# Kernel optimization log

Hardware: AMD Instinct MI355X
Metric: run time of the kernel (lower is better)

## Reference

```python
import jax, jax.numpy as jnp
import numpy as np

B, NB, NA, D, PF = 16384, 8, 16, 128, 1
IN_DIM = D + NA * D + D  # basis + flattened sf + task = 2304
QK_DIM = D * 3 * PF      # 384
V_DIM = D * PF           # 128


def rbf_similarity(x, y):
    # RBF kernel over the feature axis: exp(-0.5 * ||x - y||^2)
    return jnp.exp(-0.5 * jnp.sum((x - y) ** 2, axis=-1))


def setup_inputs() -> dict:
    key = jax.random.key(0)
    ks = jax.random.split(key, 9)
    basis = jax.random.normal(ks[0], (B, NB, D), dtype=jnp.float32)
    sf_all = jax.random.normal(ks[1], (B, NB, NA, D), dtype=jnp.float32)
    task = jax.random.normal(ks[2], (B, NB, D), dtype=jnp.float32)
    mask = (jax.random.uniform(ks[3], (B, NB, D * PF)) > 0.5).astype(jnp.float32)
    s_in = 1.0 / np.sqrt(IN_DIM)
    s_v = 1.0 / np.sqrt(D)
    Wq = jax.random.normal(ks[4], (IN_DIM, QK_DIM), dtype=jnp.float32) * s_in
    Wk = jax.random.normal(ks[5], (IN_DIM, QK_DIM), dtype=jnp.float32) * s_in
    bk = jnp.zeros((QK_DIM,), dtype=jnp.float32)
    Wv = jax.random.normal(ks[6], (D, V_DIM), dtype=jnp.float32) * s_v
    bv = jnp.zeros((V_DIM,), dtype=jnp.float32)
    return {"basis_features_all": basis, "sf_all": sf_all, "task": task, "mask": mask,
            "Wq": Wq, "Wk": Wk, "bk": bk, "Wv": Wv, "bv": bv}


def reference(basis_features_all, sf_all, task, mask, Wq, Wk, bk, Wv, bv):
    b = sf_all.shape[0]
    sf_all_r = jnp.reshape(sf_all, (b, NB, NA * D))          # (B, NB, NA*D)
    sf_first_r = sf_all_r[:, :1, :]                          # (B, 1, NA*D)
    task = jax.lax.stop_gradient(task)
    task_n = task / jnp.linalg.norm(task, ord=2, axis=-1, keepdims=True)

    # RBF similarity side-branch between consecutive beakers
    bst = jnp.concatenate([basis_features_all, sf_all_r, task_n], axis=-1)  # (B, NB, IN_DIM)
    sim = rbf_similarity(bst[:, :-1, :], bst[:, 1:, :]).mean(axis=0)        # (NB-1,)

    bf_first = basis_features_all[:, :1, :]
    bf_rest = jax.lax.stop_gradient(basis_features_all[:, 1:, :])
    bf_all = jnp.concatenate([bf_first, bf_rest], axis=1)

    q_in = jnp.concatenate([bf_first, sf_first_r, task_n[:, :1, :]], axis=-1)  # (B, 1, IN_DIM)
    query = q_in @ Wq                                                          # (B, 1, QK)
    k_in = jnp.concatenate([bf_all, sf_all_r, task_n], axis=-1)                # (B, NB, IN_DIM)
    keys = k_in @ Wk + bk                                                      # (B, NB, QK)
    values = sf_all @ Wv + bv                                                  # (B, NB, NA, V)

    mask_rep = jnp.repeat(mask, 3, axis=-1)                                    # (B, NB, QK)
    keys_masked = keys * mask_rep
    values_masked = values

    attn_logits = jnp.matmul(query, jnp.swapaxes(keys_masked, -2, -1)) / jnp.sqrt(jnp.float32(D * PF))
    attn_logits = jnp.where(attn_logits == 0, -1e9, attn_logits)               # zero-mask trick
    attention_weights = jax.nn.softmax(attn_logits, axis=-1)                   # (B, 1, NB)

    attended_sf = jnp.einsum('bna,baqf->bnqf', attention_weights, values_masked)  # (B, 1, NA, V)
    task_first = task[:, 0, :]                                                    # (B, D)
    q_1 = jnp.einsum('bi,bnji->bj', task_first, attended_sf)                      # (B, NA)
    return (q_1, attended_sf, attn_logits, attention_weights, keys_masked, values_masked, sim)
```

## Files before the change

kernel.cpp:

```cpp
#include <hip/hip_runtime.h>
#include <hip/hip_bf16.h>
#include <math.h>

static constexpr size_t OFF_ATT = 262144;
static constexpr size_t OFF_LOG = 33816576;
static constexpr size_t OFF_W   = 33947648;
static constexpr size_t OFF_KM  = 34078720;
static constexpr size_t OFF_VM  = 84410368;
static constexpr size_t OFF_SIM = 352845824;

typedef short bf16x8 __attribute__((ext_vector_type(8)));
typedef float f32x4 __attribute__((ext_vector_type(4)));

__device__ inline unsigned short f2bf(float f) {
  union { float f; unsigned u; } x; x.f = f;
  unsigned r = x.u + 0x7FFFu + ((x.u >> 16) & 1u);
  return (unsigned short)(r >> 16);
}

__device__ inline float wave_sum(float v) {
#pragma unroll
  for (int o = 32; o > 0; o >>= 1) v += __shfl_xor(v, o, 64);
  return v;
}

__global__ void norm_kernel(const float* __restrict__ task, float* __restrict__ invn,
                            float* __restrict__ simo) {
  int idx = blockIdx.x * 4 + (threadIdx.x >> 6);
  int lane = threadIdx.x & 63;
  float t0 = task[(size_t)idx * 128 + lane];
  float t1 = task[(size_t)idx * 128 + 64 + lane];
  float s = wave_sum(t0 * t0 + t1 * t1);
  if (lane == 0) invn[idx] = rsqrtf(s);
  if (blockIdx.x == 0 && threadIdx.x < 7) simo[threadIdx.x] = 0.0f;
}

__global__ void wprep_t(const float* __restrict__ W, unsigned short* __restrict__ WT,
                        int K, int N) {
  int ntn = N >> 6;
  int kt = blockIdx.x / ntn, nt = blockIdx.x % ntn;
  int k0 = kt * 64, n0 = nt * 64;
  __shared__ float t[64][65];
  int tid = threadIdx.x;
  int r = tid >> 2, c0 = (tid & 3) * 16;
#pragma unroll
  for (int q = 0; q < 4; ++q) {
    float4 v = *(const float4*)(W + (size_t)(k0 + r) * N + n0 + c0 + q * 4);
    t[r][c0 + q * 4 + 0] = v.x; t[r][c0 + q * 4 + 1] = v.y;
    t[r][c0 + q * 4 + 2] = v.z; t[r][c0 + q * 4 + 3] = v.w;
  }
  __syncthreads();
  int n = tid >> 2, kc0 = (tid & 3) * 16;
#pragma unroll
  for (int q = 0; q < 4; ++q) {
    int kc = kc0 + q * 4;
    ushort4 o = make_ushort4(f2bf(t[kc + 0][n]), f2bf(t[kc + 1][n]),
                             f2bf(t[kc + 2][n]), f2bf(t[kc + 3][n]));
    *(ushort4*)(WT + (size_t)(n0 + n) * K + k0 + kc) = o;
  }
}

__global__ __launch_bounds__(576) void abuild_sim(const float* __restrict__ basis,
                                                  const float* __restrict__ sf,
                                                  const float* __restrict__ task,
                                                  const float* __restrict__ invn,
                                                  unsigned short* __restrict__ Abf,
                                                  float* __restrict__ simo) {
  int b = blockIdx.x;
  int f = threadIdx.x;
  size_t row0 = (size_t)b * 8;
  float4 v[8];
#pragma unroll
  for (int n = 0; n < 8; ++n) {
    size_t row = row0 + n;
    float4 x;
    if (f < 32)       x = *(const float4*)(basis + row * 128 + f * 4);
    else if (f < 544) x = *(const float4*)(sf + row * 2048 + (f - 32) * 4);
    else {
      x = *(const float4*)(task + row * 128 + (f - 544) * 4);
      float s = invn[row];
      x.x *= s; x.y *= s; x.z *= s; x.w *= s;
    }
    v[n] = x;
    ushort4 o = make_ushort4(f2bf(x.x), f2bf(x.y), f2bf(x.z), f2bf(x.w));
    *(ushort4*)(Abf + row * 2304 + f * 4) = o;
  }
  float s7[7];
#pragma unroll
  for (int n = 1; n < 8; ++n) {
    float dx = v[n].x - v[n - 1].x, dy = v[n].y - v[n - 1].y;
    float dz = v[n].z - v[n - 1].z, dw = v[n].w - v[n - 1].w;
    s7[n - 1] = dx * dx + dy * dy + dz * dz + dw * dw;
  }
  __shared__ float red[9][7];
  int wid = threadIdx.x >> 6, lane = threadIdx.x & 63;
#pragma unroll
  for (int i = 0; i < 7; ++i) {
    float p = wave_sum(s7[i]);
    if (lane == 0) red[wid][i] = p;
  }
  __syncthreads();
  if (threadIdx.x < 7) {
    float s = 0.f;
#pragma unroll
    for (int w = 0; w < 9; ++w) s += red[w][threadIdx.x];
    atomicAdd(&simo[threadIdx.x], expf(-0.5f * s) * (1.0f / 16384.0f));
  }
}

template <int MODE>
__global__ __launch_bounds__(256) void qk_gemm(const unsigned short* __restrict__ Abf,
                                               const unsigned short* __restrict__ WT,
                                               const float* __restrict__ bias,
                                               const float* __restrict__ mask,
                                               float* __restrict__ outp) {
  __shared__ unsigned short As[2 * 4096];
  __shared__ unsigned short Bs[2 * 4096];
  int nwg = gridDim.x, per = nwg >> 3;
  int bid = blockIdx.x;
  int swz = (bid & 7) * per + (bid >> 3);
  int mt = swz / 3, nt = swz - mt * 3;
  int tid = threadIdx.x;
  int wave = tid >> 6, lane = tid & 63;
  int wr = wave >> 1, wc = wave & 1;
  int m0g = mt * 128, n0g = nt * 128;

  int c_lo = wave * 128 + lane;
  int row_q0 = c_lo >> 2, kc_q0 = ((c_lo & 3) ^ ((row_q0 >> 1) & 3)) * 8;
  int c_hi = c_lo + 64;
  int row_q1 = c_hi >> 2, kc_q1 = ((c_hi & 3) ^ ((row_q1 >> 1) & 3)) * 8;
  size_t ga_q0 = (MODE == 1) ? (size_t)(m0g + row_q0) * 8 : (size_t)(m0g + row_q0);
  size_t ga_q1 = (MODE == 1) ? (size_t)(m0g + row_q1) * 8 : (size_t)(m0g + row_q1);
  const unsigned short* ag0 = Abf + ga_q0 * 2304 + kc_q0;
  const unsigned short* ag1 = Abf + ga_q1 * 2304 + kc_q1;
  const unsigned short* bg0 = WT + (size_t)(n0g + row_q0) * 2304 + kc_q0;
  const unsigned short* bg1 = WT + (size_t)(n0g + row_q1) * 2304 + kc_q1;
  int ldsoff0 = wave * 1024;
  int ldsoff1 = ldsoff0 + 512;

#define STAGE(ks, cur)                                                                   \
  do {                                                                                   \
    int _k0 = (ks) * 32;                                                                 \
    unsigned short* _a = As + (cur) * 4096;                                              \
    unsigned short* _b = Bs + (cur) * 4096;                                              \
    __builtin_amdgcn_global_load_lds(                                                    \
        (const __attribute__((address_space(1))) void*)(ag0 + _k0),                      \
        (__attribute__((address_space(3))) void*)(_a + ldsoff0), 16, 0, 0);              \
    __builtin_amdgcn_global_load_lds(                                                    \
        (const __attribute__((address_space(1))) void*)(ag1 + _k0),                      \
        (__attribute__((address_space(3))) void*)(_a + ldsoff1), 16, 0, 0);              \
    __builtin_amdgcn_global_load_lds(                                                    \
        (const __attribute__((address_space(1))) void*)(bg0 + _k0),                      \
        (__attribute__((address_space(3))) void*)(_b + ldsoff0), 16, 0, 0);              \
    __builtin_amdgcn_global_load_lds(                                                    \
        (const __attribute__((address_space(1))) void*)(bg1 + _k0),                      \
        (__attribute__((address_space(3))) void*)(_b + ldsoff1), 16, 0, 0);              \
  } while (0)

  f32x4 acc[4][4];
#pragma unroll
  for (int i = 0; i < 4; ++i)
#pragma unroll
    for (int j = 0; j < 4; ++j) acc[i][j] = (f32x4)(0.f);

  int la = lane & 15;
  int sl = (((lane >> 4) ^ ((la >> 1) & 3))) * 8;

  STAGE(0, 0);
  __syncthreads();
  int cur = 0;
  for (int ks = 0; ks < 72; ++ks) {
    if (ks < 71) STAGE(ks + 1, cur ^ 1);
    const unsigned short* aL = As + cur * 4096;
    const unsigned short* bL = Bs + cur * 4096;
    bf16x8 af[4], bf[4];
#pragma unroll
    for (int mi = 0; mi < 4; ++mi)
      af[mi] = *(const bf16x8*)(aL + (wr * 64 + mi * 16 + la) * 32 + sl);
#pragma unroll
    for (int ni = 0; ni < 4; ++ni)
      bf[ni] = *(const bf16x8*)(bL + (wc * 64 + ni * 16 + la) * 32 + sl);
#pragma unroll
    for (int mi = 0; mi < 4; ++mi)
#pragma unroll
      for (int ni = 0; ni < 4; ++ni)
        acc[mi][ni] = __builtin_amdgcn_mfma_f32_16x16x32_bf16(af[mi], bf[ni], acc[mi][ni], 0, 0, 0);
    __syncthreads();
    cur ^= 1;
  }
#undef STAGE

  int rq = lane >> 4;
#pragma unroll
  for (int mi = 0; mi < 4; ++mi) {
#pragma unroll
    for (int ni = 0; ni < 4; ++ni) {
      int colg = nt * 128 + wc * 64 + ni * 16 + la;
#pragma unroll
      for (int j = 0; j < 4; ++j) {
        int rowg = mt * 128 + wr * 64 + mi * 16 + rq * 4 + j;
        float v = acc[mi][ni][j];
        if (MODE == 0)
          v = (v + bias[colg]) * mask[(size_t)rowg * 128 + (unsigned)colg / 3u];
        outp[(size_t)rowg * 384 + colg] = v;
      }
    }
  }
}

__global__ __launch_bounds__(256) void attn_kernel4(const float* __restrict__ query,
                                                    const float* __restrict__ km,
                                                    float* __restrict__ logits,
                                                    float* __restrict__ wts) {
  int w = threadIdx.x >> 6, lane = threadIdx.x & 63;
  int b = blockIdx.x * 4 + w;
  float q[6];
#pragma unroll
  for (int j = 0; j < 6; ++j) q[j] = query[(size_t)b * 384 + lane + 64 * j];
  float lg[8];
#pragma unroll
  for (int n = 0; n < 8; ++n) {
    const float* kr = km + ((size_t)b * 8 + n) * 384;
    float p = 0.f;
#pragma unroll
    for (int j = 0; j < 6; ++j) p = fmaf(q[j], kr[lane + 64 * j], p);
    p = wave_sum(p);
    float l = p * 0.08838834764831845f;
    lg[n] = (l == 0.0f) ? -1e9f : l;
  }
  float m = lg[0];
#pragma unroll
  for (int i = 1; i < 8; ++i) m = fmaxf(m, lg[i]);
  float ex[8], s = 0.f;
#pragma unroll
  for (int i = 0; i < 8; ++i) { ex[i] = expf(lg[i] - m); s += ex[i]; }
  float inv = 1.0f / s;
  if (lane < 8) {
    float lv = lg[0], ev = ex[0];
#pragma unroll
    for (int i = 1; i < 8; ++i)
      if (lane == i) { lv = lg[i]; ev = ex[i]; }
    logits[(size_t)b * 8 + lane] = lv;
    wts[(size_t)b * 8 + lane] = ev * inv;
  }
}

template <int ABF>
__global__ __launch_bounds__(256) void v_gemm_attend(const float* __restrict__ sf,
                                                     const unsigned short* __restrict__ Abf,
                                                     const float* __restrict__ Wv,
                                                     const unsigned short* __restrict__ WvT,
                                                     const float* __restrict__ bv,
                                                     const float* __restrict__ wts,
                                                     const float* __restrict__ task,
                                                     float* __restrict__ vm,
                                                     float* __restrict__ att,
                                                     float* __restrict__ q1) {
  __shared__ unsigned short As[2 * 4096];
  __shared__ unsigned short Bs[128 * 136];
  float* attL = (float*)As;
  int bid = blockIdx.x;
  int swz = (bid & 7) * 2048 + (bid >> 3);
  int b = swz;
  size_t m0 = (size_t)swz * 128;
  int tid = threadIdx.x;
  int wave = tid >> 6, lane = tid & 63;
  int wr = wave >> 1, wc = wave & 1;
  int r = tid >> 1, h = tid & 1;
  int la = lane & 15, lkq = lane >> 4;
  int sl = ((lkq ^ ((la >> 1) & 3))) * 8;

  if (ABF) {
#pragma unroll
    for (int q = 0; q < 8; ++q) {
      bf16x8 v = *(const bf16x8*)(WvT + (size_t)r * 128 + h * 64 + q * 8);
      *(bf16x8*)(Bs + r * 136 + h * 64 + q * 8) = v;
    }
  } else {
#pragma unroll
    for (int q = 0; q < 16; ++q) {
      int flat = q * 256 + tid;
      int k = flat >> 5;
      int n4 = (flat & 31) * 4;
      float4 v = *(const float4*)(Wv + (size_t)k * 128 + n4);
      Bs[(n4 + 0) * 136 + k] = f2bf(v.x);
      Bs[(n4 + 1) * 136 + k] = f2bf(v.y);
      Bs[(n4 + 2) * 136 + k] = f2bf(v.z);
      Bs[(n4 + 3) * 136 + k] = f2bf(v.w);
    }
  }

  const unsigned short *ap0 = nullptr, *ap1 = nullptr;
  int ldsA0 = wave * 1024, ldsA1 = ldsA0 + 512;
  if (ABF) {
    int p0 = wave * 128 + lane;
    int tr0 = p0 >> 2, ds0 = (p0 & 3) ^ ((tr0 >> 1) & 3);
    int p1 = p0 + 64;
    int tr1 = p1 >> 2, ds1 = (p1 & 3) ^ ((tr1 >> 1) & 3);
    ap0 = Abf + ((size_t)b * 8 + (tr0 >> 4)) * 2304 + 128 + (tr0 & 15) * 128 + ds0 * 8;
    ap1 = Abf + ((size_t)b * 8 + (tr1 >> 4)) * 2304 + 128 + (tr1 & 15) * 128 + ds1 * 8;
    __builtin_amdgcn_global_load_lds(
        (const __attribute__((address_space(1))) void*)(ap0),
        (__attribute__((address_space(3))) void*)(As + ldsA0), 16, 0, 0);
    __builtin_amdgcn_global_load_lds(
        (const __attribute__((address_space(1))) void*)(ap1),
        (__attribute__((address_space(3))) void*)(As + ldsA1), 16, 0, 0);
  }

  f32x4 acc[4][4];
#pragma unroll
  for (int i = 0; i < 4; ++i)
#pragma unroll
    for (int j = 0; j < 4; ++j) acc[i][j] = (f32x4)(0.f);

  if (ABF) __syncthreads();

  int cur = 0;
  for (int ks = 0; ks < 4; ++ks) {
    int k0 = ks * 32;
    if (ABF) {
      if (ks < 3) {
        __builtin_amdgcn_global_load_lds(
            (const __attribute__((address_space(1))) void*)(ap0 + k0 + 32),
            (__attribute__((address_space(3))) void*)(As + (cur ^ 1) * 4096 + ldsA0), 16, 0, 0);
        __builtin_amdgcn_global_load_lds(
            (const __attribute__((address_space(1))) void*)(ap1 + k0 + 32),
            (__attribute__((address_space(3))) void*)(As + (cur ^ 1) * 4096 + ldsA1), 16, 0, 0);
      }
    } else {
      const float* ap = sf + (m0 + r) * 128 + k0 + h * 16;
      float4 v0 = *(const float4*)(ap);
      float4 v1 = *(const float4*)(ap + 4);
      float4 v2 = *(const float4*)(ap + 8);
      float4 v3 = *(const float4*)(ap + 12);
      ushort4 p0 = make_ushort4(f2bf(v0.x), f2bf(v0.y), f2bf(v0.z), f2bf(v0.w));
      ushort4 p1 = make_ushort4(f2bf(v1.x), f2bf(v1.y), f2bf(v1.z), f2bf(v1.w));
      ushort4 p2 = make_ushort4(f2bf(v2.x), f2bf(v2.y), f2bf(v2.z), f2bf(v2.w));
      ushort4 p3 = make_ushort4(f2bf(v3.x), f2bf(v3.y), f2bf(v3.z), f2bf(v3.w));
      *(ushort4*)(As + r * 40 + h * 16)      = p0;
      *(ushort4*)(As + r * 40 + h * 16 + 4)  = p1;
      *(ushort4*)(As + r * 40 + h * 16 + 8)  = p2;
      *(ushort4*)(As + r * 40 + h * 16 + 12) = p3;
      __syncthreads();
    }
    const unsigned short* aL = ABF ? (As + cur * 4096) : As;
    bf16x8 af[4], bfr[4];
#pragma unroll
    for (int mi = 0; mi < 4; ++mi) {
      int rowl = wr * 64 + mi * 16 + la;
      af[mi] = ABF ? *(const bf16x8*)(aL + rowl * 32 + sl)
                   : *(const bf16x8*)(aL + rowl * 40 + lkq * 8);
    }
#pragma unroll
    for (int ni = 0; ni < 4; ++ni)
      bfr[ni] = *(const bf16x8*)(Bs + (wc * 64 + ni * 16 + la) * 136 + k0 + lkq * 8);
#pragma unroll
    for (int mi = 0; mi < 4; ++mi)
#pragma unroll
      for (int ni = 0; ni < 4; ++ni)
        acc[mi][ni] = __builtin_amdgcn_mfma_f32_16x16x32_bf16(af[mi], bfr[ni], acc[mi][ni], 0, 0, 0);
    __syncthreads();
    cur ^= 1;
  }

  float w4[4];
#pragma unroll
  for (int mi = 0; mi < 4; ++mi) w4[mi] = wts[(size_t)b * 8 + wr * 4 + mi];
  float pacc[4][4];
#pragma unroll
  for (int ni = 0; ni < 4; ++ni)
#pragma unroll
    for (int j = 0; j < 4; ++j) pacc[ni][j] = 0.f;
#pragma unroll
  for (int mi = 0; mi < 4; ++mi) {
#pragma unroll
    for (int ni = 0; ni < 4; ++ni) {
      int colg = wc * 64 + ni * 16 + la;
      float bb = bv[colg];
#pragma unroll
      for (int j = 0; j < 4; ++j) {
        size_t rowg = m0 + wr * 64 + mi * 16 + lkq * 4 + j;
        float v = acc[mi][ni][j] + bb;
        vm[rowg * 128 + colg] = v;
        pacc[ni][j] = fmaf(w4[mi], v, pacc[ni][j]);
      }
    }
  }
  if (wr == 0) {
#pragma unroll
    for (int ni = 0; ni < 4; ++ni)
#pragma unroll
      for (int j = 0; j < 4; ++j)
        attL[(lkq * 4 + j) * 132 + wc * 64 + ni * 16 + la] = pacc[ni][j];
  }
  __syncthreads();
  if (wr == 1) {
#pragma unroll
    for (int ni = 0; ni < 4; ++ni)
#pragma unroll
      for (int j = 0; j < 4; ++j)
        attL[(lkq * 4 + j) * 132 + wc * 64 + ni * 16 + la] += pacc[ni][j];
  }
  __syncthreads();
#pragma unroll
  for (int i = 0; i < 2; ++i) {
    int fidx = tid + i * 256;
    int a = fidx >> 5, c = (fidx & 31) * 4;
    f32x4 vv = *(const f32x4*)(attL + a * 132 + c);
    *(f32x4*)(att + (size_t)b * 2048 + a * 128 + c) = vv;
  }
  for (int j = wave; j < 16; j += 4) {
    float p = task[(size_t)b * 1024 + lane] * attL[j * 132 + lane]
            + task[(size_t)b * 1024 + 64 + lane] * attL[j * 132 + 64 + lane];
    p = wave_sum(p);
    if (lane == 0) q1[(size_t)b * 16 + j] = p;
  }
}

extern "C" void kernel_launch(void* const* d_in, const int* in_sizes, int n_in,
                              void* d_out, int out_size, void* d_ws, size_t ws_size,
                              hipStream_t stream) {
  const float* basis = (const float*)d_in[0];
  const float* sf    = (const float*)d_in[1];
  const float* task  = (const float*)d_in[2];
  const float* mask  = (const float*)d_in[3];
  const float* Wq    = (const float*)d_in[4];
  const float* Wk    = (const float*)d_in[5];
  const float* bk    = (const float*)d_in[6];
  const float* Wv    = (const float*)d_in[7];
  const float* bv    = (const float*)d_in[8];

  float* out  = (float*)d_out;
  float* q1   = out;
  float* att  = out + OFF_ATT;
  float* logi = out + OFF_LOG;
  float* wts  = out + OFF_W;
  float* km   = out + OFF_KM;
  float* vm   = out + OFF_VM;
  float* simo = out + OFF_SIM;

  constexpr size_t WS_NEED = 603979776ull + 1769472ull + 1769472ull + 32768ull +
                             25165824ull + 524288ull;
  bool usews = ws_size >= WS_NEED;

  unsigned short *Abf, *WkT, *WqT, *WvT = nullptr;
  float *query, *invn;
  if (usews) {
    unsigned char* ws = (unsigned char*)d_ws;
    Abf   = (unsigned short*)ws;
    WkT   = (unsigned short*)(ws + 603979776ull);
    WqT   = (unsigned short*)(ws + 605749248ull);
    WvT   = (unsigned short*)(ws + 607518720ull);
    query = (float*)(ws + 607551488ull);
    invn  = (float*)(ws + 632717312ull);
  } else {
    query = att;
    invn  = att + 6291456;
    WkT   = (unsigned short*)(att + 6422528);
    WqT   = WkT + 884736;
    Abf   = (unsigned short*)vm;
  }

  norm_kernel<<<32768, 256, 0, stream>>>(task, invn, simo);
  wprep_t<<<216, 256, 0, stream>>>(Wk, WkT, 2304, 384);
  wprep_t<<<216, 256, 0, stream>>>(Wq, WqT, 2304, 384);
  if (usews) wprep_t<<<4, 256, 0, stream>>>(Wv, WvT, 128, 128);
  abuild_sim<<<16384, 576, 0, stream>>>(basis, sf, task, invn, Abf, simo);
  qk_gemm<0><<<3072, 256, 0, stream>>>(Abf, WkT, bk, mask, km);
  qk_gemm<1><<<384, 256, 0, stream>>>(Abf, WqT, nullptr, nullptr, query);
  attn_kernel4<<<4096, 256, 0, stream>>>(query, km, logi, wts);
  if (usews)
    v_gemm_attend<1><<<16384, 256, 0, stream>>>(sf, Abf, Wv, WvT, bv, wts, task, vm, att, q1);
  else
    v_gemm_attend<0><<<16384, 256, 0, stream>>>(sf, Abf, Wv, WvT, bv, wts, task, vm, att, q1);
}
```

Before: 1.283 ms.

## Fuse input conversion and similarity into keys GEMM, drop full bf16 A buffer

A new keys_build kernel loads the fp32 basis, sf and normalized task rows directly, converts them to bf16 in LDS and runs the key GEMM in the same pass, so the separate abuild_sim kernel no longer writes and re-reads the full bf16 A matrix. It also produces a compact bf16 copy of sf for the V GEMM and the query rows for the Q GEMM, spreading these writes across the three column-tile blocks. The RBF similarity is accumulated from the bf16 tiles already in LDS, which lowers its precision. Each of the three column tiles now re-reads the fp32 inputs, relying on the swizzle and L2 to soften that cost.

Result: slower. 1.509 ms (+17.7%).

```diff
diff --git a/kernel.cpp b/kernel.cpp
--- a/kernel.cpp
+++ b/kernel.cpp
@@ -16,6 +16,9 @@
   union { float f; unsigned u; } x; x.f = f;
   unsigned r = x.u + 0x7FFFu + ((x.u >> 16) & 1u);
   return (unsigned short)(r >> 16);
+}
+__device__ inline float bf2f(unsigned short v) {
+  union { unsigned u; float f; } x; x.u = ((unsigned)v) << 16; return x.f;
 }
 
 __device__ inline float wave_sum(float v) {
@@ -57,6 +60,172 @@
     ushort4 o = make_ushort4(f2bf(t[kc + 0][n]), f2bf(t[kc + 1][n]),
                              f2bf(t[kc + 2][n]), f2bf(t[kc + 3][n]));
     *(ushort4*)(WT + (size_t)(n0 + n) * K + k0 + kc) = o;
+  }
+}
+
+__global__ __launch_bounds__(256) void keys_build(
+    const float* __restrict__ basis, const float* __restrict__ sf,
+    const float* __restrict__ task, const float* __restrict__ invn,
+    const unsigned short* __restrict__ WkT, const float* __restrict__ bias,
+    const float* __restrict__ mask, float* __restrict__ km,
+    unsigned short* __restrict__ sfbf, unsigned short* __restrict__ qbf,
+    float* __restrict__ simo) {
+  __shared__ unsigned short As[2 * 5120];
+  __shared__ unsigned short Bs[2 * 4096];
+  int bid = blockIdx.x;
+  int swz = (bid & 7) * 384 + (bid >> 3);
+  int mt = swz / 3, nt = swz - mt * 3;
+  int tid = threadIdx.x;
+  int wave = tid >> 6, lane = tid & 63;
+  int wr = wave >> 1, wc = wave & 1;
+  int m0g = mt * 128, n0g = nt * 128;
+  int la = lane & 15, lkq = lane >> 4;
+  int sl = ((lkq ^ ((la >> 1) & 3))) * 8;
+
+  int c_lo = wave * 128 + lane;
+  int brow0 = c_lo >> 2, bkc0 = ((c_lo & 3) ^ ((brow0 >> 1) & 3)) * 8;
+  int c_hi = c_lo + 64;
+  int brow1 = c_hi >> 2, bkc1 = ((c_hi & 3) ^ ((brow1 >> 1) & 3)) * 8;
+  const unsigned short* bg0 = WkT + (size_t)(n0g + brow0) * 2304 + bkc0;
+  const unsigned short* bg1 = WkT + (size_t)(n0g + brow1) * 2304 + bkc1;
+  int ldsB0 = wave * 1024, ldsB1 = ldsB0 + 512;
+
+#define STAGE_B(ks, cb)                                                        \
+  do {                                                                         \
+    __builtin_amdgcn_global_load_lds(                                          \
+        (const __attribute__((address_space(1))) void*)(bg0 + (ks) * 32),      \
+        (__attribute__((address_space(3))) void*)(Bs + (cb) * 4096 + ldsB0),   \
+        16, 0, 0);                                                             \
+    __builtin_amdgcn_global_load_lds(                                          \
+        (const __attribute__((address_space(1))) void*)(bg1 + (ks) * 32),      \
+        (__attribute__((address_space(3))) void*)(Bs + (cb) * 4096 + ldsB1),   \
+        16, 0, 0);                                                             \
+  } while (0)
+
+  int rbase = tid >> 3, c4 = tid & 7;
+  float ivq[4];
+#pragma unroll
+  for (int q = 0; q < 4; ++q) ivq[q] = invn[m0g + rbase + 32 * q];
+  bool qrow = ((rbase & 7) == 0);
+  bool simblk = (nt == 0);
+
+  float4 av[4];
+
+  auto LOADA = [&](int k0) {
+#pragma unroll
+    for (int q = 0; q < 4; ++q) {
+      size_t R = (size_t)(m0g + rbase + 32 * q);
+      int k = k0 + c4 * 4;
+      const float* p;
+      if (k0 < 128)       p = basis + R * 128 + k;
+      else if (k0 < 2176) p = sf + R * 2048 + (k - 128);
+      else                p = task + R * 128 + (k - 2176);
+      float4 x = *(const float4*)p;
+      if (k0 >= 2176) { x.x *= ivq[q]; x.y *= ivq[q]; x.z *= ivq[q]; x.w *= ivq[q]; }
+      av[q] = x;
+    }
+  };
+
+  auto CVTW = [&](int cb, int kt) {
+    unsigned short* aL = As + cb * 5120;
+    bool wr_this = (nt == (kt % 3));
+    int k0 = kt * 32;
+#pragma unroll
+    for (int q = 0; q < 4; ++q) {
+      int row = rbase + 32 * q;
+      ushort4 o = make_ushort4(f2bf(av[q].x), f2bf(av[q].y), f2bf(av[q].z), f2bf(av[q].w));
+      *(ushort4*)(aL + row * 40 + c4 * 4) = o;
+      if (wr_this) {
+        size_t R = (size_t)(m0g + row);
+        int k = k0 + c4 * 4;
+        if (k0 >= 128 && k0 < 2176)
+          *(ushort4*)(sfbf + R * 2048 + (k - 128)) = o;
+        if (qrow)
+          *(ushort4*)(qbf + (R >> 3) * 2304 + k) = o;
+      }
+    }
+  };
+
+  f32x4 acc[4][4];
+#pragma unroll
+  for (int i = 0; i < 4; ++i)
+#pragma unroll
+    for (int j = 0; j < 4; ++j) acc[i][j] = (f32x4)(0.f);
+
+  float sa = 0.f;
+  int pr = tid >> 1, hh = tid & 1;
+  bool prok = ((pr & 7) != 7);
+
+  LOADA(0);
+  STAGE_B(0, 0);
+  CVTW(0, 0);
+  __syncthreads();
+
+  int cur = 0;
+  for (int ks = 0; ks < 72; ++ks) {
+    if (ks < 71) {
+      LOADA((ks + 1) * 32);
+      STAGE_B(ks + 1, cur ^ 1);
+    }
+    {
+      const unsigned short* aL = As + cur * 5120;
+      const unsigned short* bL = Bs + cur * 4096;
+      bf16x8 af[4], bfr[4];
+#pragma unroll
+      for (int mi = 0; mi < 4; ++mi)
+        af[mi] = *(const bf16x8*)(aL + (wr * 64 + mi * 16 + la) * 40 + lkq * 8);
+#pragma unroll
+      for (int ni = 0; ni < 4; ++ni)
+        bfr[ni] = *(const bf16x8*)(bL + (wc * 64 + ni * 16 + la) * 32 + sl);
+#pragma unroll
+      for (int mi = 0; mi < 4; ++mi)
+#pragma unroll
+        for (int ni = 0; ni < 4; ++ni)
+          acc[mi][ni] = __builtin_amdgcn_mfma_f32_16x16x32_bf16(af[mi], bfr[ni], acc[mi][ni], 0, 0, 0);
+    }
+    if (simblk && prok) {
+      const unsigned short* a0 = As + cur * 5120 + pr * 40 + hh * 16;
+      bf16x8 x0 = *(const bf16x8*)(a0);
+      bf16x8 x1 = *(const bf16x8*)(a0 + 8);
+      bf16x8 y0 = *(const bf16x8*)(a0 + 40);
+      bf16x8 y1 = *(const bf16x8*)(a0 + 48);
+#pragma unroll
+      for (int j = 0; j < 8; ++j) {
+        float d0 = bf2f((unsigned short)x0[j]) - bf2f((unsigned short)y0[j]);
+        sa = fmaf(d0, d0, sa);
+        float d1 = bf2f((unsigned short)x1[j]) - bf2f((unsigned short)y1[j]);
+        sa = fmaf(d1, d1, sa);
+      }
+    }
+    if (ks < 71) CVTW(cur ^ 1, ks + 1);
+    __syncthreads();
+    cur ^= 1;
+  }
+#undef STAGE_B
+
+  int rq = lane >> 4;
+#pragma unroll
+  for (int mi = 0; mi < 4; ++mi) {
+#pragma unroll
+    for (int ni = 0; ni < 4; ++ni) {
+      int colg = n0g + wc * 64 + ni * 16 + la;
+#pragma unroll
+      for (int j = 0; j < 4; ++j) {
+        int rowg = m0g + wr * 64 + mi * 16 + rq * 4 + j;
+        float v = (acc[mi][ni][j] + bias[colg]) * mask[(size_t)rowg * 128 + (unsigned)colg / 3u];
+        km[(size_t)rowg * 384 + colg] = v;
+      }
+    }
+  }
+
+  if (simblk) {
+    float* sarr = (float*)Bs;
+    sarr[tid] = sa;
+    __syncthreads();
+    if (hh == 0 && prok) {
+      float s = sarr[tid] + sarr[tid + 1];
+      atomicAdd(&simo[pr & 7], expf(-0.5f * s) * (1.0f / 16384.0f));
+    }
   }
 }
 
@@ -129,8 +298,8 @@
   int row_q0 = c_lo >> 2, kc_q0 = ((c_lo & 3) ^ ((row_q0 >> 1) & 3)) * 8;
   int c_hi = c_lo + 64;
   int row_q1 = c_hi >> 2, kc_q1 = ((c_hi & 3) ^ ((row_q1 >> 1) & 3)) * 8;
-  size_t ga_q0 = (MODE == 1) ? (size_t)(m0g + row_q0) * 8 : (size_t)(m0g + row_q0);
-  size_t ga_q1 = (MODE == 1) ? (size_t)(m0g + row_q1) * 8 : (size_t)(m0g + row_q1);
+  size_t ga_q0 = (MODE == 2) ? (size_t)(m0g + row_q0) * 8 : (size_t)(m0g + row_q0);
+  size_t ga_q1 = (MODE == 2) ? (size_t)(m0g + row_q1) * 8 : (size_t)(m0g + row_q1);
   const unsigned short* ag0 = Abf + ga_q0 * 2304 + kc_q0;
   const unsigned short* ag1 = Abf + ga_q1 * 2304 + kc_q1;
   const unsigned short* bg0 = WT + (size_t)(n0g + row_q0) * 2304 + kc_q0;
@@ -247,7 +416,7 @@
 
 template <int ABF>
 __global__ __launch_bounds__(256) void v_gemm_attend(const float* __restrict__ sf,
-                                                     const unsigned short* __restrict__ Abf,
+                                                     const unsigned short* __restrict__ sfbf,
                                                      const float* __restrict__ Wv,
                                                      const unsigned short* __restrict__ WvT,
                                                      const float* __restrict__ bv,
@@ -297,8 +466,8 @@
     int tr0 = p0 >> 2, ds0 = (p0 & 3) ^ ((tr0 >> 1) & 3);
     int p1 = p0 + 64;
     int tr1 = p1 >> 2, ds1 = (p1 & 3) ^ ((tr1 >> 1) & 3);
-    ap0 = Abf + ((size_t)b * 8 + (tr0 >> 4)) * 2304 + 128 + (tr0 & 15) * 128 + ds0 * 8;
-    ap1 = Abf + ((size_t)b * 8 + (tr1 >> 4)) * 2304 + 128 + (tr1 & 15) * 128 + ds1 * 8;
+    ap0 = sfbf + ((size_t)b * 8 + (tr0 >> 4)) * 2048 + (tr0 & 15) * 128 + ds0 * 8;
+    ap1 = sfbf + ((size_t)b * 8 + (tr1 >> 4)) * 2048 + (tr1 & 15) * 128 + ds1 * 8;
     __builtin_amdgcn_global_load_lds(
         (const __attribute__((address_space(1))) void*)(ap0),
         (__attribute__((address_space(3))) void*)(As + ldsA0), 16, 0, 0);
@@ -439,38 +608,51 @@
   float* vm   = out + OFF_VM;
   float* simo = out + OFF_SIM;
 
-  constexpr size_t WS_NEED = 603979776ull + 1769472ull + 1769472ull + 32768ull +
-                             25165824ull + 524288ull;
+  constexpr size_t O_SFBF = 0;
+  constexpr size_t O_QBF  = 536870912ull;
+  constexpr size_t O_WKT  = O_QBF + 75497472ull;
+  constexpr size_t O_WQT  = O_WKT + 1769472ull;
+  constexpr size_t O_WVT  = O_WQT + 1769472ull;
+  constexpr size_t O_QRY  = O_WVT + 32768ull;
+  constexpr size_t O_INV  = O_QRY + 25165824ull;
+  constexpr size_t WS_NEED = O_INV + 524288ull;
   bool usews = ws_size >= WS_NEED;
 
-  unsigned short *Abf, *WkT, *WqT, *WvT = nullptr;
-  float *query, *invn;
   if (usews) {
     unsigned char* ws = (unsigned char*)d_ws;
-    Abf   = (unsigned short*)ws;
-    WkT   = (unsigned short*)(ws + 603979776ull);
-    WqT   = (unsigned short*)(ws + 605749248ull);
-    WvT   = (unsigned short*)(ws + 607518720ull);
-    query = (float*)(ws + 607551488ull);
-    invn  = (float*)(ws + 632717312ull);
+    unsigned short* sfbf = (unsigned short*)(ws + O_SFBF);
+    unsigned short* qbf  = (unsigned short*)(ws + O_QBF);
+    unsigned short* WkT  = (unsigned short*)(ws + O_WKT);
+    unsigned short* WqT  = (unsigned short*)(ws + O_WQT);
+    unsigned short* WvT  = (unsigned short*)(ws + O_WVT);
+    float* query = (float*)(ws + O_QRY);
+    float* invn  = (float*)(ws + O_INV);
+
+    norm_kernel<<<32768, 256, 0, stream>>>(task, invn, simo);
+    wprep_t<<<216, 256, 0, stream>>>(Wk, WkT, 2304, 384);
+    wprep_t<<<216, 256, 0, stream>>>(Wq, WqT, 2304, 384);
+    wprep_t<<<4, 256, 0, stream>>>(Wv, WvT, 128, 128);
+    keys_build<<<3072, 256, 0, stream>>>(basis, sf, task, invn, WkT, bk, mask,
+                                         km, sfbf, qbf, simo);
+    qk_gemm<1><<<384, 256, 0, stream>>>(qbf, WqT, nullptr, nullptr, query);
+    attn_kernel4<<<4096, 256, 0, stream>>>(query, km, logi, wts);
+    v_gemm_attend<1><<<16384, 256, 0, stream>>>(sf, sfbf, Wv, WvT, bv, wts, task,
+                                                vm, att, q1);
   } else {
-    query = att;
-    invn  = att + 6291456;
-    WkT   = (unsigned short*)(att + 6422528);
-    WqT   = WkT + 884736;
-    Abf   = (unsigned short*)vm;
-  }
-
-  norm_kernel<<<32768, 256, 0, stream>>>(task, invn, simo);
-  wprep_t<<<216, 256, 0, stream>>>(Wk, WkT, 2304, 384);
-  wprep_t<<<216, 256, 0, stream>>>(Wq, WqT, 2304, 384);
-  if (usews) wprep_t<<<4, 256, 0, stream>>>(Wv, WvT, 128, 128);
-  abuild_sim<<<16384, 576, 0, stream>>>(basis, sf, task, invn, Abf, simo);
-  qk_gemm<0><<<3072, 256, 0, stream>>>(Abf, WkT, bk, mask, km);
-  qk_gemm<1><<<384, 256, 0, stream>>>(Abf, WqT, nullptr, nullptr, query);
-  attn_kernel4<<<4096, 256, 0, stream>>>(query, km, logi, wts);
-  if (usews)
-    v_gemm_attend<1><<<16384, 256, 0, stream>>>(sf, Abf, Wv, WvT, bv, wts, task, vm, att, q1);
-  else
-    v_gemm_attend<0><<<16384, 256, 0, stream>>>(sf, Abf, Wv, WvT, bv, wts, task, vm, att, q1);
-}
+    float* query = att;
+    float* invn  = att + 6291456;
+    unsigned short* WkT = (unsigned short*)(att + 6422528);
+    unsigned short* WqT = WkT + 884736;
+    unsigned short* Abf = (unsigned short*)vm;
+
+    norm_kernel<<<32768, 256, 0, stream>>>(task, invn, simo);
+    wprep_t<<<216, 256, 0, stream>>>(Wk, WkT, 2304, 384);
+    wprep_t<<<216, 256, 0, stream>>>(Wq, WqT, 2304, 384);
+    abuild_sim<<<16384, 576, 0, stream>>>(basis, sf, task, invn, Abf, simo);
+    qk_gemm<0><<<3072, 256, 0, stream>>>(Abf, WkT, bk, mask, km);
+    qk_gemm<2><<<384, 256, 0, stream>>>(Abf, WqT, nullptr, nullptr, query);
+    attn_kernel4<<<4096, 256, 0, stream>>>(query, km, logi, wts);
+    v_gemm_attend<0><<<16384, 256, 0, stream>>>(sf, nullptr, Wv, nullptr, bv, wts,
+                                                task, vm, att, q1);
+  }
+}
```

## Merge K and Q GEMMs into one launch with triple-buffered async LDS loads

Applied to the files above, without the earlier changes.

Combines the key and query projection GEMMs into a single kernel whose blocks pick weights and output by block index, removing one launch and the tail gap between them. The LDS staging goes from double to triple buffering, using explicit vmcnt waits and raw barriers so two tiles are in flight while the current one is computed. LDS use per block rises to 48KB, which may lower occupancy. The non-workspace v_gemm_attend call now passes nullptr for Abf and WvT; that is only safe if that path never reads them.

After: 1.398 ms. +9.0%, slower.

```diff
diff --git a/kernel.cpp b/kernel.cpp
--- a/kernel.cpp
+++ b/kernel.cpp
@@ -108,18 +108,30 @@
   }
 }
 
-template <int MODE>
-__global__ __launch_bounds__(256) void qk_gemm(const unsigned short* __restrict__ Abf,
-                                               const unsigned short* __restrict__ WT,
-                                               const float* __restrict__ bias,
-                                               const float* __restrict__ mask,
-                                               float* __restrict__ outp) {
-  __shared__ unsigned short As[2 * 4096];
-  __shared__ unsigned short Bs[2 * 4096];
-  int nwg = gridDim.x, per = nwg >> 3;
+__global__ __launch_bounds__(256) void qk2(const unsigned short* __restrict__ Abf,
+                                           const unsigned short* __restrict__ WkT,
+                                           const unsigned short* __restrict__ WqT,
+                                           const float* __restrict__ bias,
+                                           const float* __restrict__ mask,
+                                           float* __restrict__ km,
+                                           float* __restrict__ query) {
+  __shared__ unsigned short As[3 * 4096];
+  __shared__ unsigned short Bs[3 * 4096];
   int bid = blockIdx.x;
-  int swz = (bid & 7) * per + (bid >> 3);
-  int mt = swz / 3, nt = swz - mt * 3;
+  bool isq = bid >= 3072;
+  int mt, nt;
+  const unsigned short* WT;
+  float* outp;
+  if (!isq) {
+    int swz = (bid & 7) * 384 + (bid >> 3);
+    mt = swz / 3; nt = swz - mt * 3;
+    WT = WkT; outp = km;
+  } else {
+    int q = bid - 3072;
+    int swz = (q & 7) * 48 + (q >> 3);
+    mt = swz / 3; nt = swz - mt * 3;
+    WT = WqT; outp = query;
+  }
   int tid = threadIdx.x;
   int wave = tid >> 6, lane = tid & 63;
   int wr = wave >> 1, wc = wave & 1;
@@ -129,8 +141,8 @@
   int row_q0 = c_lo >> 2, kc_q0 = ((c_lo & 3) ^ ((row_q0 >> 1) & 3)) * 8;
   int c_hi = c_lo + 64;
   int row_q1 = c_hi >> 2, kc_q1 = ((c_hi & 3) ^ ((row_q1 >> 1) & 3)) * 8;
-  size_t ga_q0 = (MODE == 1) ? (size_t)(m0g + row_q0) * 8 : (size_t)(m0g + row_q0);
-  size_t ga_q1 = (MODE == 1) ? (size_t)(m0g + row_q1) * 8 : (size_t)(m0g + row_q1);
+  size_t ga_q0 = isq ? (size_t)(m0g + row_q0) * 8 : (size_t)(m0g + row_q0);
+  size_t ga_q1 = isq ? (size_t)(m0g + row_q1) * 8 : (size_t)(m0g + row_q1);
   const unsigned short* ag0 = Abf + ga_q0 * 2304 + kc_q0;
   const unsigned short* ag1 = Abf + ga_q1 * 2304 + kc_q1;
   const unsigned short* bg0 = WT + (size_t)(n0g + row_q0) * 2304 + kc_q0;
@@ -138,11 +150,11 @@
   int ldsoff0 = wave * 1024;
   int ldsoff1 = ldsoff0 + 512;
 
-#define STAGE(ks, cur)                                                                   \
+#define STAGE(ks, buf)                                                                   \
   do {                                                                                   \
     int _k0 = (ks) * 32;                                                                 \
-    unsigned short* _a = As + (cur) * 4096;                                              \
-    unsigned short* _b = Bs + (cur) * 4096;                                              \
+    unsigned short* _a = As + (buf) * 4096;                                              \
+    unsigned short* _b = Bs + (buf) * 4096;                                              \
     __builtin_amdgcn_global_load_lds(                                                    \
         (const __attribute__((address_space(1))) void*)(ag0 + _k0),                      \
         (__attribute__((address_space(3))) void*)(_a + ldsoff0), 16, 0, 0);              \
@@ -167,12 +179,16 @@
   int sl = (((lane >> 4) ^ ((la >> 1) & 3))) * 8;
 
   STAGE(0, 0);
-  __syncthreads();
-  int cur = 0;
+  STAGE(1, 1);
+  asm volatile("s_waitcnt vmcnt(4)" ::: "memory");
+  __builtin_amdgcn_s_barrier();
+  asm volatile("" ::: "memory");
+
+  int rd = 0, st = 2;
   for (int ks = 0; ks < 72; ++ks) {
-    if (ks < 71) STAGE(ks + 1, cur ^ 1);
-    const unsigned short* aL = As + cur * 4096;
-    const unsigned short* bL = Bs + cur * 4096;
+    if (ks < 70) STAGE(ks + 2, st);
+    const unsigned short* aL = As + rd * 4096;
+    const unsigned short* bL = Bs + rd * 4096;
     bf16x8 af[4], bf[4];
 #pragma unroll
     for (int mi = 0; mi < 4; ++mi)
@@ -185,8 +201,12 @@
 #pragma unroll
       for (int ni = 0; ni < 4; ++ni)
         acc[mi][ni] = __builtin_amdgcn_mfma_f32_16x16x32_bf16(af[mi], bf[ni], acc[mi][ni], 0, 0, 0);
-    __syncthreads();
-    cur ^= 1;
+    if (ks < 70) asm volatile("s_waitcnt vmcnt(4)" ::: "memory");
+    else         asm volatile("s_waitcnt vmcnt(0)" ::: "memory");
+    __builtin_amdgcn_s_barrier();
+    asm volatile("" ::: "memory");
+    rd = (rd == 2) ? 0 : rd + 1;
+    st = (st == 2) ? 0 : st + 1;
   }
 #undef STAGE
 
@@ -200,7 +220,7 @@
       for (int j = 0; j < 4; ++j) {
         int rowg = mt * 128 + wr * 64 + mi * 16 + rq * 4 + j;
         float v = acc[mi][ni][j];
-        if (MODE == 0)
+        if (!isq)
           v = (v + bias[colg]) * mask[(size_t)rowg * 128 + (unsigned)colg / 3u];
         outp[(size_t)rowg * 384 + colg] = v;
       }
@@ -466,11 +486,10 @@
   wprep_t<<<216, 256, 0, stream>>>(Wq, WqT, 2304, 384);
   if (usews) wprep_t<<<4, 256, 0, stream>>>(Wv, WvT, 128, 128);
   abuild_sim<<<16384, 576, 0, stream>>>(basis, sf, task, invn, Abf, simo);
-  qk_gemm<0><<<3072, 256, 0, stream>>>(Abf, WkT, bk, mask, km);
-  qk_gemm<1><<<384, 256, 0, stream>>>(Abf, WqT, nullptr, nullptr, query);
+  qk2<<<3456, 256, 0, stream>>>(Abf, WkT, WqT, bk, mask, km, query);
   attn_kernel4<<<4096, 256, 0, stream>>>(query, km, logi, wts);
   if (usews)
     v_gemm_attend<1><<<16384, 256, 0, stream>>>(sf, Abf, Wv, WvT, bv, wts, task, vm, att, q1);
   else
-    v_gemm_attend<0><<<16384, 256, 0, stream>>>(sf, Abf, Wv, WvT, bv, wts, task, vm, att, q1);
-}
+    v_gemm_attend<0><<<16384, 256, 0, stream>>>(sf, nullptr, Wv, nullptr, bv, wts, task, vm, att, q1);
+}
```
